# Kernel tuning notes

Measured on AMD Instinct MI355X. Metric: run time of the kernel, lower is better.

## Reference

```python
import jax, jax.numpy as jnp
import numpy as np

B, Q, P, HID, H, KV, D = 2, 1024, 3072, 4096, 32, 8, 128
G = H // KV          # GQA group size
EPS = 1e-6
ROPE_THETA = 1e6


def setup_inputs() -> dict:
    key = jax.random.key(0)
    ks = jax.random.split(key, 8)
    hidden_states = jax.random.normal(ks[0], (B, Q, HID), jnp.float32)
    # real RoPE tables for positions [P, P+Q) (extend phase)
    pos = jnp.arange(P, P + Q, dtype=jnp.float32)
    inv_freq = 1.0 / (ROPE_THETA ** (jnp.arange(0, D, 2, dtype=jnp.float32) / D))
    freqs = pos[:, None] * inv_freq[None, :]            # [Q, D/2]
    emb = jnp.concatenate([freqs, freqs], axis=-1)       # [Q, D]
    cos = jnp.broadcast_to(jnp.cos(emb)[None], (B, Q, D)).astype(jnp.float32)
    sin = jnp.broadcast_to(jnp.sin(emb)[None], (B, Q, D)).astype(jnp.float32)
    k_cache = jax.random.normal(ks[1], (B, KV, P, D), jnp.float32)
    v_cache = jax.random.normal(ks[2], (B, KV, P, D), jnp.float32)
    s = 0.02
    Wq = jax.random.normal(ks[3], (HID, H * D), jnp.float32) * s
    Wk = jax.random.normal(ks[4], (HID, KV * D), jnp.float32) * s
    Wv = jax.random.normal(ks[5], (HID, KV * D), jnp.float32) * s
    Wo = jax.random.normal(ks[6], (H * D, HID), jnp.float32) * s
    q_norm_w = jnp.ones((D,), jnp.float32)
    k_norm_w = jnp.ones((D,), jnp.float32)
    return dict(hidden_states=hidden_states, cos=cos, sin=sin,
                k_cache=k_cache, v_cache=v_cache,
                Wq=Wq, Wk=Wk, Wv=Wv, Wo=Wo,
                q_norm_w=q_norm_w, k_norm_w=k_norm_w)


def _rmsnorm(x, w):
    var = jnp.mean(x * x, axis=-1, keepdims=True)
    return x * jax.lax.rsqrt(var + EPS) * w


def _rotate_half(x):
    x1, x2 = jnp.split(x, 2, axis=-1)
    return jnp.concatenate([-x2, x1], axis=-1)


def _rope(x, cos, sin):
    # x: [B, h, Q, D]; cos/sin: [B, Q, D] -> broadcast over heads
    c = cos[:, None, :, :]
    s = sin[:, None, :, :]
    return x * c + _rotate_half(x) * s


def reference(hidden_states, cos, sin, k_cache, v_cache,
              Wq, Wk, Wv, Wo, q_norm_w, k_norm_w):
    # projections
    q = (hidden_states @ Wq).reshape(B, Q, H, D)
    k = (hidden_states @ Wk).reshape(B, Q, KV, D)
    v = (hidden_states @ Wv).reshape(B, Q, KV, D)
    # per-head RMSNorm on q and k
    q = _rmsnorm(q, q_norm_w)
    k = _rmsnorm(k, k_norm_w)
    # [B, heads, Q, D]
    q = q.transpose(0, 2, 1, 3)
    k = k.transpose(0, 2, 1, 3)
    v = v.transpose(0, 2, 1, 3)
    q = _rope(q, cos, sin)
    k = _rope(k, cos, sin)
    # extend: concat cached prefix KV with new KV -> kv_len = P + Q
    K = jnp.concatenate([k_cache, k], axis=2)   # [B, KV, P+Q, D]
    V = jnp.concatenate([v_cache, v], axis=2)
    qg = q.reshape(B, KV, G, Q, D)
    scale = 1.0 / jnp.sqrt(jnp.float32(D))
    scores = jnp.einsum('bkgqd,bksd->bkgqs', qg, K) * scale  # [B,KV,G,Q,P+Q]
    # causal mask offset by prefix: query i sees keys <= P + i
    key_idx = jnp.arange(P + Q)
    mask = key_idx[None, :] <= (P + jnp.arange(Q))[:, None]  # [Q, P+Q]
    scores = jnp.where(mask[None, None, None], scores, jnp.float32(-1e30))
    attn = jax.nn.softmax(scores, axis=-1)
    out = jnp.einsum('bkgqs,bksd->bkgqd', attn, V)           # [B,KV,G,Q,D]
    out = out.reshape(B, H, Q, D).transpose(0, 2, 1, 3).reshape(B, Q, H * D)
    return out @ Wo
```

## Files before the change

### kernel.cpp

```cpp
#include <hip/hip_runtime.h>
#include <hip/hip_bf16.h>

#define B_ 2
#define Q_ 1024
#define P_ 3072
#define HID_ 4096
#define H_ 32
#define KV_ 8
#define D_ 128
#define S_ 4096
#define NQKV 6144
#define QSCALE 0.1275174432f

typedef __attribute__((ext_vector_type(4))) float f32x4;
typedef __attribute__((ext_vector_type(8))) unsigned short u16x8;
typedef __attribute__((ext_vector_type(4))) unsigned short u16x4;
typedef __attribute__((ext_vector_type(8))) __bf16 bf16x8;

__device__ __forceinline__ unsigned short f2bf(float f){
  unsigned u = __builtin_bit_cast(unsigned, f);
  unsigned r = (u + 0x7FFFu + ((u >> 16) & 1u)) >> 16;
  return (unsigned short)r;
}
__device__ __forceinline__ unsigned pk2bf(float lo, float hi){
  unsigned r;
  asm("v_cvt_pk_bf16_f32 %0, %1, %2" : "=v"(r) : "v"(lo), "v"(hi));
  return r;
}
__device__ __forceinline__ f32x4 mfma16(u16x8 a, u16x8 b, f32x4 c){
  return __builtin_amdgcn_mfma_f32_16x16x32_bf16(
      __builtin_bit_cast(bf16x8, a), __builtin_bit_cast(bf16x8, b), c, 0, 0, 0);
}
typedef const __attribute__((address_space(1))) void* gp1_t;
typedef __attribute__((address_space(3))) void* lp3_t;
__device__ __forceinline__ void gl16(const unsigned short* g, unsigned short* l){
  __builtin_amdgcn_global_load_lds((gp1_t)g, (lp3_t)l, 16, 0, 0);
}

__global__ __launch_bounds__(256) void convert_hs(
    const float* __restrict__ X, unsigned short* __restrict__ Hh, int total4){
  for(int i4 = blockIdx.x * 256 + threadIdx.x; i4 < total4; i4 += gridDim.x * 256){
    long i = (long)i4 * 4;
    float4 x = *(const float4*)(X + i);
    *(u16x4*)(Hh + i) = (u16x4){f2bf(x.x), f2bf(x.y), f2bf(x.z), f2bf(x.w)};
  }
}

__global__ __launch_bounds__(256) void convert_wt(
    const float* __restrict__ W, unsigned short* __restrict__ Th, int ldn, int n_off){
  __shared__ float tile[64][65];
  int k0 = blockIdx.y * 64, n0 = blockIdx.x * 64;
  int tid = threadIdx.x;
  int r = tid >> 4, c = (tid & 15) * 4;
  #pragma unroll
  for(int j = 0; j < 4; ++j){
    float4 v = *(const float4*)(W + (long)(k0 + r + j*16) * ldn + n0 + c);
    tile[r + j*16][c] = v.x; tile[r + j*16][c+1] = v.y;
    tile[r + j*16][c+2] = v.z; tile[r + j*16][c+3] = v.w;
  }
  __syncthreads();
  #pragma unroll
  for(int j = 0; j < 4; ++j){
    int n = r + j*16;
    long o = (long)(n_off + n0 + n) * 4096 + k0 + c;
    *(u16x4*)(Th + o) = (u16x4){f2bf(tile[c][n]), f2bf(tile[c+1][n]),
                                f2bf(tile[c+2][n]), f2bf(tile[c+3][n])};
  }
}

__global__ __launch_bounds__(256) void cache_k(
    const float* __restrict__ kc, unsigned short* __restrict__ Kb){
  const int PD = P_ * D_;
  const long SD = (long)S_ * D_;
  int total4 = (B_ * KV_ * PD) >> 2;
  for(int i4 = blockIdx.x * 256 + threadIdx.x; i4 < total4; i4 += gridDim.x * 256){
    long i = (long)i4 * 4;
    int bkv = (int)(i / PD);
    int rem = (int)(i - (long)bkv * PD);
    long dst = (long)bkv * SD + rem;
    float4 k4 = *(const float4*)(kc + i);
    *(u16x4*)(Kb + dst) = (u16x4){f2bf(k4.x), f2bf(k4.y), f2bf(k4.z), f2bf(k4.w)};
  }
}

__global__ __launch_bounds__(256) void cache_vt(
    const float* __restrict__ vc, unsigned short* __restrict__ VT){
  __shared__ unsigned short T[128][72];
  int bkv = blockIdx.y;
  int s0 = blockIdx.x * 64;
  int tid = threadIdx.x;
  int r = tid >> 2, dblk = (tid & 3) * 32;
  const float* src = vc + ((long)bkv * P_ + s0 + r) * 128 + dblk;
  #pragma unroll
  for(int u = 0; u < 8; ++u){
    float4 v = *(const float4*)(src + u*4);
    T[dblk + u*4 + 0][r] = f2bf(v.x);
    T[dblk + u*4 + 1][r] = f2bf(v.y);
    T[dblk + u*4 + 2][r] = f2bf(v.z);
    T[dblk + u*4 + 3][r] = f2bf(v.w);
  }
  __syncthreads();
  int d = tid >> 1, sh = (tid & 1) * 32;
  unsigned short* dst = VT + ((long)bkv * 128 + d) * S_ + s0 + sh;
  #pragma unroll
  for(int u = 0; u < 4; ++u){
    u16x8 v;
    #pragma unroll
    for(int j = 0; j < 8; ++j) v[j] = T[d][sh + u*8 + j];
    *(u16x8*)(dst + u*8) = v;
  }
}

__global__ __launch_bounds__(128) void maxw(
    const float* __restrict__ qw, const float* __restrict__ kw, float* __restrict__ M){
  __shared__ float sa[2], sb[2];
  int t = threadIdx.x;
  float a = fabsf(qw[t]), b = fabsf(kw[t]);
  #pragma unroll
  for(int o = 32; o; o >>= 1){
    a = fmaxf(a, __shfl_xor(a, o));
    b = fmaxf(b, __shfl_xor(b, o));
  }
  if((t & 63) == 0){ sa[t >> 6] = a; sb[t >> 6] = b; }
  __syncthreads();
  if(t == 0){
    float mq = fmaxf(sa[0], sa[1]), mk = fmaxf(sb[0], sb[1]);
    M[0] = 128.0f * QSCALE * mq * mk * 1.01f + 0.25f;
  }
}

__global__ __launch_bounds__(256) void gemm_bf16(
    const unsigned short* __restrict__ Ag, const unsigned short* __restrict__ Bg,
    float* __restrict__ C, int nbx, int ldc){
  __shared__ __align__(16) unsigned short sA[4096], sB[4096];
  int tid = threadIdx.x;
  int nwg = nbx * 16;
  int lin = blockIdx.x;
  int cpx = nwg >> 3;
  int swz = (lin & 7) * cpx + (lin >> 3);
  int bx = swz % nbx, by = swz / nbx;
  int m0 = by * 128, n0 = bx * 128;
  int lane = tid & 63, w = tid >> 6;
  int lr = lane & 15, lg = lane >> 4;
  int wm = (w >> 1) * 64, wn = (w & 1) * 64;
  int rowi = w * 16 + (lane >> 2);
  int cchunk = ((lane & 3) ^ ((lane >> 3) & 3)) << 3;
  const unsigned short* aP = Ag + (long)(m0 + rowi) * 4096 + cchunk;
  const unsigned short* bP = Bg + (long)(n0 + rowi) * 4096 + cchunk;
  const int step2 = 64 * 4096;
  unsigned short* dA = sA + w * 512;
  unsigned short* dB = sB + w * 512;
  int rdcol = (lg * 8) ^ (((lr >> 1) & 3) << 3);
  f32x4 zero = {0.f,0.f,0.f,0.f};
  f32x4 acc[4][4];
  #pragma unroll
  for(int mi=0;mi<4;++mi)
    #pragma unroll
    for(int ni=0;ni<4;++ni) acc[mi][ni] = zero;

  for(int kt = 0; kt < 128; ++kt){
    int kk = kt * 32;
    __syncthreads();
    gl16(aP + kk, dA);  gl16(aP + step2 + kk, dA + 2048);
    gl16(bP + kk, dB);  gl16(bP + step2 + kk, dB + 2048);
    __syncthreads();
    u16x8 ah[4];
    #pragma unroll
    for(int mi = 0; mi < 4; ++mi)
      ah[mi] = *(const u16x8*)(sA + (wm + mi*16 + lr) * 32 + rdcol);
    #pragma unroll
    for(int ni = 0; ni < 4; ++ni){
      u16x8 bh = *(const u16x8*)(sB + (wn + ni*16 + lr) * 32 + rdcol);
      #pragma unroll
      for(int mi = 0; mi < 4; ++mi)
        acc[mi][ni] = mfma16(ah[mi], bh, acc[mi][ni]);
    }
  }
  #pragma unroll
  for(int mi = 0; mi < 4; ++mi)
    #pragma unroll
    for(int r = 0; r < 4; ++r){
      long rowoff = (long)(m0 + wm + mi*16 + lg*4 + r) * ldc + n0 + wn + lr;
      #pragma unroll
      for(int ni = 0; ni < 4; ++ni)
        C[rowoff + ni*16] = acc[mi][ni][r];
    }
}

__global__ __launch_bounds__(256) void pp_q(
    const float* __restrict__ Craw, const float* __restrict__ cosb,
    const float* __restrict__ sinb, const float* __restrict__ qw,
    unsigned short* __restrict__ Qb){
  int rid = blockIdx.x * 4 + (threadIdx.x >> 6);
  int lane = threadIdx.x & 63;
  int b = rid >> 15;
  int rem = rid & 32767;
  int q = rem >> 5;
  int h = rem & 31;
  long rowoff = (long)(b * Q_ + q) * NQKV + h * 128;
  float x1 = Craw[rowoff + lane];
  float x2 = Craw[rowoff + 64 + lane];
  float ss = x1*x1 + x2*x2;
  for(int o = 32; o; o >>= 1) ss += __shfl_xor(ss, o);
  float norm = rsqrtf(ss * (1.0f/128.0f) + 1e-6f);
  float xn1 = x1 * norm * qw[lane];
  float xn2 = x2 * norm * qw[64 + lane];
  long co = (long)(b * Q_ + q) * 128;
  float c1 = cosb[co + lane],      s1 = sinb[co + lane];
  float c2 = cosb[co + 64 + lane], s2 = sinb[co + 64 + lane];
  float o1 = (xn1 * c1 - xn2 * s1) * QSCALE;
  float o2 = (xn2 * c2 + xn1 * s2) * QSCALE;
  long dst = ((long)(b * H_ + h) * Q_ + q) * 128;
  Qb[dst + lane] = f2bf(o1);
  Qb[dst + 64 + lane] = f2bf(o2);
}

__global__ __launch_bounds__(256) void pp_kv(
    const float* __restrict__ Craw, const float* __restrict__ cosb,
    const float* __restrict__ sinb, const float* __restrict__ kw,
    unsigned short* __restrict__ Kb, unsigned short* __restrict__ VT){
  int rid = blockIdx.x * 4 + (threadIdx.x >> 6);
  int lane = threadIdx.x & 63;
  int b = rid >> 13;
  int rem = rid & 8191;
  int q = rem >> 3;
  int kv = rem & 7;
  int bkv = b * KV_ + kv;
  long rowoff = (long)(b * Q_ + q) * NQKV;
  float x1 = Craw[rowoff + 4096 + kv*128 + lane];
  float x2 = Craw[rowoff + 4096 + kv*128 + 64 + lane];
  float ss = x1*x1 + x2*x2;
  for(int o = 32; o; o >>= 1) ss += __shfl_xor(ss, o);
  float norm = rsqrtf(ss * (1.0f/128.0f) + 1e-6f);
  float xn1 = x1 * norm * kw[lane];
  float xn2 = x2 * norm * kw[64 + lane];
  long co = (long)(b * Q_ + q) * 128;
  float c1 = cosb[co + lane],      s1 = sinb[co + lane];
  float c2 = cosb[co + 64 + lane], s2 = sinb[co + 64 + lane];
  long dst = ((long)bkv * S_ + P_ + q) * 128;
  Kb[dst + lane]      = f2bf(xn1 * c1 - xn2 * s1);
  Kb[dst + 64 + lane] = f2bf(xn2 * c2 + xn1 * s2);
  float v1 = Craw[rowoff + 5120 + kv*128 + lane];
  float v2 = Craw[rowoff + 5120 + kv*128 + 64 + lane];
  VT[((long)bkv * 128 + lane) * S_ + P_ + q]      = f2bf(v1);
  VT[((long)bkv * 128 + 64 + lane) * S_ + P_ + q] = f2bf(v2);
}

#define KVB 32
#define PSL 40
__global__ __launch_bounds__(256) void attn(
    const unsigned short* __restrict__ Qg, const unsigned short* __restrict__ Kg,
    const unsigned short* __restrict__ VTg, const float* __restrict__ Mp,
    float* __restrict__ po, float* __restrict__ pl){
  __shared__ __align__(16) unsigned short Ks[2][KVB*128];
  __shared__ __align__(16) unsigned short Vs[2][128*KVB];
  __shared__ __align__(16) unsigned short Ps[4][32*PSL];
  int tid = threadIdx.x;
  int qb = blockIdx.x >> 1, sp = blockIdx.x & 1;
  int b = blockIdx.z, h = blockIdx.y, q0 = qb * 128;
  int kvh = h >> 2;
  int w = tid >> 6, lane = tid & 63, lr = lane & 15, lg = lane >> 4;
  int q0w = q0 + w * 32;
  float Mv = Mp[0];
  u16x8 qh[2][4];
  #pragma unroll
  for(int mi = 0; mi < 2; ++mi){
    long qbase = ((long)(b * H_ + h) * Q_ + q0w + mi*16 + lr) * 128;
    #pragma unroll
    for(int c = 0; c < 4; ++c)
      qh[mi][c] = *(const u16x8*)(Qg + qbase + c*32 + lg*8);
  }
  f32x4 minit = {-Mv, -Mv, -Mv, -Mv};
  f32x4 zero = {0.f,0.f,0.f,0.f};
  f32x4 o[2][8];
  #pragma unroll
  for(int mi = 0; mi < 2; ++mi)
    #pragma unroll
    for(int i = 0; i < 8; ++i) o[mi][i] = zero;
  float l[2] = {0.f, 0.f};
  long kb  = (long)(b * KV_ + kvh) * S_ * 128;
  long vb0 = (long)(b * KV_ + kvh) * 128 * (long)S_;
  int T = 100 + 4 * qb;
  int half = T >> 1;
  int t0 = sp ? half : 0;
  int t1 = sp ? T : half;
  int koff[2], voff[2], ldst[2];
  #pragma unroll
  for(int i = 0; i < 2; ++i){
    int L = (w*2 + i)*64 + lane;
    ldst[i] = L * 8;
    int r = L >> 4, c8 = (L & 15) ^ (r & 7);
    koff[i] = r*128 + c8*8;
    int d = L >> 2, sc = (L & 3) ^ (d & 3) ^ ((d >> 2) & 3);
    voff[i] = d*S_ + sc*8;
  }
  {
    const unsigned short* kg = Kg + kb + (long)t0 * (KVB*128);
    const unsigned short* vg = VTg + vb0 + t0 * KVB;
    #pragma unroll
    for(int i = 0; i < 2; ++i){
      gl16(kg + koff[i], &Ks[t0 & 1][ldst[i]]);
      gl16(vg + voff[i], &Vs[t0 & 1][ldst[i]]);
    }
  }
  __syncthreads();

  int lr7 = lr & 7;
  for(int t = t0; t < t1; ++t){
    int cur = t & 1;
    if(t + 1 < t1){
      int s1 = (t + 1) * KVB;
      const unsigned short* kg = Kg + kb + (long)s1 * 128;
      const unsigned short* vg = VTg + vb0 + s1;
      #pragma unroll
      for(int i = 0; i < 2; ++i){
        gl16(kg + koff[i], &Ks[cur^1][ldst[i]]);
        gl16(vg + voff[i], &Vs[cur^1][ldst[i]]);
      }
    }
    int s0 = t * KVB;
    if(s0 <= P_ + q0w + 31){
      f32x4 pacc[2][2];
      pacc[0][0] = minit; pacc[0][1] = minit; pacc[1][0] = minit; pacc[1][1] = minit;
      #pragma unroll
      for(int c = 0; c < 4; ++c)
        #pragma unroll
        for(int ni = 0; ni < 2; ++ni){
          u16x8 kh = *(const u16x8*)(&Ks[cur][(ni*16 + lr)*128 + (((c*4 + lg) ^ lr7) << 3)]);
          pacc[0][ni] = mfma16(kh, qh[0][c], pacc[0][ni]);
          pacc[1][ni] = mfma16(kh, qh[1][c], pacc[1][ni]);
        }
      if(s0 + KVB - 1 > P_ + q0w){
        #pragma unroll
        for(int mi = 0; mi < 2; ++mi){
          int qrow = q0w + mi*16 + lr;
          #pragma unroll
          for(int ni = 0; ni < 2; ++ni)
            #pragma unroll
            for(int r = 0; r < 4; ++r){
              int skey = s0 + ni*16 + lg*4 + r;
              if(skey > P_ + qrow) pacc[mi][ni][r] = -1e30f;
            }
        }
      }
      #pragma unroll
      for(int mi = 0; mi < 2; ++mi){
        float rs = 0.f;
        #pragma unroll
        for(int ni = 0; ni < 2; ++ni){
          float p0 = exp2f(pacc[mi][ni][0]);
          float p1 = exp2f(pacc[mi][ni][1]);
          float p2 = exp2f(pacc[mi][ni][2]);
          float p3 = exp2f(pacc[mi][ni][3]);
          rs += (p0 + p1) + (p2 + p3);
          uint2 pw; pw.x = pk2bf(p0, p1); pw.y = pk2bf(p2, p3);
          *(uint2*)(&Ps[w][(mi*16 + lr)*PSL + ni*16 + lg*4]) = pw;
        }
        l[mi] += rs;
      }
      u16x8 pa0 = *(const u16x8*)(&Ps[w][lr*PSL + lg*8]);
      u16x8 pa1 = *(const u16x8*)(&Ps[w][(16 + lr)*PSL + lg*8]);
      #pragma unroll
      for(int ni = 0; ni < 8; ++ni){
        int d = ni*16 + lr;
        int scs = lg ^ (lr & 3) ^ ((lr >> 2) & 3);
        u16x8 vbf = *(const u16x8*)(&Vs[cur][d*32 + (scs << 3)]);
        o[0][ni] = mfma16(pa0, vbf, o[0][ni]);
        o[1][ni] = mfma16(pa1, vbf, o[1][ni]);
      }
    }
    __syncthreads();
  }
  int bh = b * H_ + h;
  #pragma unroll
  for(int mi = 0; mi < 2; ++mi){
    float lt = l[mi];
    lt += __shfl_xor(lt, 16);
    lt += __shfl_xor(lt, 32);
    #pragma unroll
    for(int r = 0; r < 4; ++r){
      int qrow = q0w + mi*16 + lg*4 + r;
      long obase = ((long)(sp*64 + bh) * Q_ + qrow) * 128;
      #pragma unroll
      for(int ni = 0; ni < 8; ++ni)
        po[obase + ni*16 + lr] = o[mi][ni][r];
    }
    if(lane < 16)
      pl[(sp*64 + bh) * Q_ + q0w + mi*16 + lane] = lt;
  }
}

__global__ __launch_bounds__(256) void combine(
    const float* __restrict__ po, const float* __restrict__ pl,
    unsigned short* __restrict__ OH){
  int idx = blockIdx.x * 256 + threadIdx.x;
  int row = idx >> 5;
  int d4 = (idx & 31) * 4;
  int bh = row >> 10, q = row & 1023;
  int b = bh >> 5, h = bh & 31;
  float lsum = pl[bh*1024 + q] + pl[65536 + bh*1024 + q];
  float inv = 1.0f / lsum;
  float4 a = *(const float4*)(po + (long)row*128 + d4);
  float4 c = *(const float4*)(po + 8388608L + (long)row*128 + d4);
  u16x4 r = { f2bf((a.x + c.x) * inv), f2bf((a.y + c.y) * inv),
              f2bf((a.z + c.z) * inv), f2bf((a.w + c.w) * inv) };
  *(u16x4*)(OH + ((long)(b*1024 + q))*4096 + h*128 + d4) = r;
}

extern "C" void kernel_launch(void* const* d_in, const int* in_sizes, int n_in,
                              void* d_out, int out_size, void* d_ws, size_t ws_size,
                              hipStream_t stream){
  const float* hs   = (const float*)d_in[0];
  const float* cosb = (const float*)d_in[1];
  const float* sinb = (const float*)d_in[2];
  const float* kc   = (const float*)d_in[3];
  const float* vc   = (const float*)d_in[4];
  const float* Wq   = (const float*)d_in[5];
  const float* Wk   = (const float*)d_in[6];
  const float* Wv   = (const float*)d_in[7];
  const float* Wo   = (const float*)d_in[8];
  const float* qw   = (const float*)d_in[9];
  const float* kw   = (const float*)d_in[10];
  char* ws = (char*)d_ws;
  float* Craw          = (float*)ws;
  unsigned short* OH   = (unsigned short*)ws;
  float* PL            = (float*)(ws + 16777216);
  float* MW            = (float*)(ws + 17301504);
  unsigned short* WTh  = (unsigned short*)(ws + 50331648);
  unsigned short* WoTh = (unsigned short*)(ws + 50331648);
  float* PO            = (float*)(ws + 83886080);
  unsigned short* AH   = (unsigned short*)(ws + 150994944);
  unsigned short* QB   = (unsigned short*)(ws + 150994944);
  unsigned short* KB   = (unsigned short*)(ws + 184549376);
  unsigned short* VT   = (unsigned short*)(ws + 218103808);
  float* Out = (float*)d_out;

  convert_hs<<<dim3(2048), dim3(256), 0, stream>>>(hs, AH, (B_*Q_*HID_)/4);
  convert_wt<<<dim3(64,64), dim3(256), 0, stream>>>(Wq, WTh, 4096, 0);
  convert_wt<<<dim3(16,64), dim3(256), 0, stream>>>(Wk, WTh, 1024, 4096);
  convert_wt<<<dim3(16,64), dim3(256), 0, stream>>>(Wv, WTh, 1024, 5120);
  cache_k<<<dim3(2048), dim3(256), 0, stream>>>(kc, KB);
  cache_vt<<<dim3(48, 16), dim3(256), 0, stream>>>(vc, VT);
  gemm_bf16<<<dim3(768), dim3(256), 0, stream>>>(AH, WTh, Craw, 48, NQKV);
  pp_q<<<dim3(16384), dim3(256), 0, stream>>>(Craw, cosb, sinb, qw, QB);
  pp_kv<<<dim3(4096), dim3(256), 0, stream>>>(Craw, cosb, sinb, kw, KB, VT);
  maxw<<<dim3(1), dim3(128), 0, stream>>>(qw, kw, MW);
  convert_wt<<<dim3(64,64), dim3(256), 0, stream>>>(Wo, WoTh, 4096, 0);
  attn<<<dim3(16, 32, 2), dim3(256), 0, stream>>>(QB, KB, VT, MW, PO, PL);
  combine<<<dim3(8192), dim3(256), 0, stream>>>(PO, PL, OH);
  gemm_bf16<<<dim3(512), dim3(256), 0, stream>>>(OH, WoTh, Out, 32, 4096);
}
```

Baseline: 537.0 us.

## Merge prep kernels, enlarge attention query tile, add MFMA priority hints

Merges the hidden-state and K-cache conversions into one kernel, converts all four weight matrices in a single launch, and fuses the Q and KV post-processing kernels, cutting the launch count. The attention kernel now handles 64 query rows per wave (256 per block), so each K/V tile in shared memory serves twice as many queries, and it sets launch bounds for 2 blocks per CU. s_setprio hints are placed around the MFMA sections in both the GEMM and attention kernels. The workspace layout is repacked so that Wo can be converted early without clobbering other buffers. The larger attention tile raises register pressure and halves the grid, which may reduce occupancy and worsen the balance of the causal work.

```diff
diff --git a/kernel.cpp b/kernel.cpp
--- a/kernel.cpp
+++ b/kernel.cpp
@@ -37,19 +37,41 @@
   __builtin_amdgcn_global_load_lds((gp1_t)g, (lp3_t)l, 16, 0, 0);
 }
 
-__global__ __launch_bounds__(256) void convert_hs(
-    const float* __restrict__ X, unsigned short* __restrict__ Hh, int total4){
-  for(int i4 = blockIdx.x * 256 + threadIdx.x; i4 < total4; i4 += gridDim.x * 256){
-    long i = (long)i4 * 4;
-    float4 x = *(const float4*)(X + i);
-    *(u16x4*)(Hh + i) = (u16x4){f2bf(x.x), f2bf(x.y), f2bf(x.z), f2bf(x.w)};
-  }
-}
-
-__global__ __launch_bounds__(256) void convert_wt(
-    const float* __restrict__ W, unsigned short* __restrict__ Th, int ldn, int n_off){
+#define N1_ 2097152
+#define N2_ 1572864
+__global__ __launch_bounds__(256) void prep(
+    const float* __restrict__ hs, const float* __restrict__ kc,
+    unsigned short* __restrict__ AH, unsigned short* __restrict__ Kb){
+  const int PD = P_ * D_;
+  const long SD = (long)S_ * D_;
+  for(int i4 = blockIdx.x * 256 + threadIdx.x; i4 < N1_ + N2_; i4 += gridDim.x * 256){
+    if(i4 < N1_){
+      long i = (long)i4 * 4;
+      float4 x = *(const float4*)(hs + i);
+      *(u16x4*)(AH + i) = (u16x4){f2bf(x.x), f2bf(x.y), f2bf(x.z), f2bf(x.w)};
+    } else {
+      long i = (long)(i4 - N1_) * 4;
+      int bkv = (int)(i / PD);
+      int rem = (int)(i - (long)bkv * PD);
+      long dst = (long)bkv * SD + rem;
+      float4 k4 = *(const float4*)(kc + i);
+      *(u16x4*)(Kb + dst) = (u16x4){f2bf(k4.x), f2bf(k4.y), f2bf(k4.z), f2bf(k4.w)};
+    }
+  }
+}
+
+__global__ __launch_bounds__(256) void convert_w(
+    const float* __restrict__ Wq, const float* __restrict__ Wk,
+    const float* __restrict__ Wv, const float* __restrict__ Wo,
+    unsigned short* __restrict__ WT, unsigned short* __restrict__ WoT){
   __shared__ float tile[64][65];
-  int k0 = blockIdx.y * 64, n0 = blockIdx.x * 64;
+  int x = blockIdx.x;
+  const float* W; int ldn, n_off; unsigned short* dst; int n0;
+  if(x < 64)      { W = Wq; ldn = 4096; n_off = 0;    dst = WT;  n0 = x * 64; }
+  else if(x < 80) { W = Wk; ldn = 1024; n_off = 4096; dst = WT;  n0 = (x-64) * 64; }
+  else if(x < 96) { W = Wv; ldn = 1024; n_off = 5120; dst = WT;  n0 = (x-80) * 64; }
+  else            { W = Wo; ldn = 4096; n_off = 0;    dst = WoT; n0 = (x-96) * 64; }
+  int k0 = blockIdx.y * 64;
   int tid = threadIdx.x;
   int r = tid >> 4, c = (tid & 15) * 4;
   #pragma unroll
@@ -63,23 +85,8 @@
   for(int j = 0; j < 4; ++j){
     int n = r + j*16;
     long o = (long)(n_off + n0 + n) * 4096 + k0 + c;
-    *(u16x4*)(Th + o) = (u16x4){f2bf(tile[c][n]), f2bf(tile[c+1][n]),
-                                f2bf(tile[c+2][n]), f2bf(tile[c+3][n])};
-  }
-}
-
-__global__ __launch_bounds__(256) void cache_k(
-    const float* __restrict__ kc, unsigned short* __restrict__ Kb){
-  const int PD = P_ * D_;
-  const long SD = (long)S_ * D_;
-  int total4 = (B_ * KV_ * PD) >> 2;
-  for(int i4 = blockIdx.x * 256 + threadIdx.x; i4 < total4; i4 += gridDim.x * 256){
-    long i = (long)i4 * 4;
-    int bkv = (int)(i / PD);
-    int rem = (int)(i - (long)bkv * PD);
-    long dst = (long)bkv * SD + rem;
-    float4 k4 = *(const float4*)(kc + i);
-    *(u16x4*)(Kb + dst) = (u16x4){f2bf(k4.x), f2bf(k4.y), f2bf(k4.z), f2bf(k4.w)};
+    *(u16x4*)(dst + o) = (u16x4){f2bf(tile[c][n]), f2bf(tile[c+1][n]),
+                                 f2bf(tile[c+2][n]), f2bf(tile[c+3][n])};
   }
 }
 
@@ -168,6 +175,7 @@
     #pragma unroll
     for(int mi = 0; mi < 4; ++mi)
       ah[mi] = *(const u16x8*)(sA + (wm + mi*16 + lr) * 32 + rdcol);
+    __builtin_amdgcn_s_setprio(1);
     #pragma unroll
     for(int ni = 0; ni < 4; ++ni){
       u16x8 bh = *(const u16x8*)(sB + (wn + ni*16 + lr) * 32 + rdcol);
@@ -175,6 +183,7 @@
       for(int mi = 0; mi < 4; ++mi)
         acc[mi][ni] = mfma16(ah[mi], bh, acc[mi][ni]);
     }
+    __builtin_amdgcn_s_setprio(0);
   }
   #pragma unroll
   for(int mi = 0; mi < 4; ++mi)
@@ -187,84 +196,81 @@
     }
 }
 
-__global__ __launch_bounds__(256) void pp_q(
+__global__ __launch_bounds__(256) void pp_qkv(
     const float* __restrict__ Craw, const float* __restrict__ cosb,
     const float* __restrict__ sinb, const float* __restrict__ qw,
-    unsigned short* __restrict__ Qb){
-  int rid = blockIdx.x * 4 + (threadIdx.x >> 6);
-  int lane = threadIdx.x & 63;
-  int b = rid >> 15;
-  int rem = rid & 32767;
-  int q = rem >> 5;
-  int h = rem & 31;
-  long rowoff = (long)(b * Q_ + q) * NQKV + h * 128;
-  float x1 = Craw[rowoff + lane];
-  float x2 = Craw[rowoff + 64 + lane];
-  float ss = x1*x1 + x2*x2;
-  for(int o = 32; o; o >>= 1) ss += __shfl_xor(ss, o);
-  float norm = rsqrtf(ss * (1.0f/128.0f) + 1e-6f);
-  float xn1 = x1 * norm * qw[lane];
-  float xn2 = x2 * norm * qw[64 + lane];
-  long co = (long)(b * Q_ + q) * 128;
-  float c1 = cosb[co + lane],      s1 = sinb[co + lane];
-  float c2 = cosb[co + 64 + lane], s2 = sinb[co + 64 + lane];
-  float o1 = (xn1 * c1 - xn2 * s1) * QSCALE;
-  float o2 = (xn2 * c2 + xn1 * s2) * QSCALE;
-  long dst = ((long)(b * H_ + h) * Q_ + q) * 128;
-  Qb[dst + lane] = f2bf(o1);
-  Qb[dst + 64 + lane] = f2bf(o2);
-}
-
-__global__ __launch_bounds__(256) void pp_kv(
-    const float* __restrict__ Craw, const float* __restrict__ cosb,
-    const float* __restrict__ sinb, const float* __restrict__ kw,
+    const float* __restrict__ kw, unsigned short* __restrict__ Qb,
     unsigned short* __restrict__ Kb, unsigned short* __restrict__ VT){
   int rid = blockIdx.x * 4 + (threadIdx.x >> 6);
   int lane = threadIdx.x & 63;
-  int b = rid >> 13;
-  int rem = rid & 8191;
-  int q = rem >> 3;
-  int kv = rem & 7;
-  int bkv = b * KV_ + kv;
-  long rowoff = (long)(b * Q_ + q) * NQKV;
-  float x1 = Craw[rowoff + 4096 + kv*128 + lane];
-  float x2 = Craw[rowoff + 4096 + kv*128 + 64 + lane];
-  float ss = x1*x1 + x2*x2;
-  for(int o = 32; o; o >>= 1) ss += __shfl_xor(ss, o);
-  float norm = rsqrtf(ss * (1.0f/128.0f) + 1e-6f);
-  float xn1 = x1 * norm * kw[lane];
-  float xn2 = x2 * norm * kw[64 + lane];
-  long co = (long)(b * Q_ + q) * 128;
-  float c1 = cosb[co + lane],      s1 = sinb[co + lane];
-  float c2 = cosb[co + 64 + lane], s2 = sinb[co + 64 + lane];
-  long dst = ((long)bkv * S_ + P_ + q) * 128;
-  Kb[dst + lane]      = f2bf(xn1 * c1 - xn2 * s1);
-  Kb[dst + 64 + lane] = f2bf(xn2 * c2 + xn1 * s2);
-  float v1 = Craw[rowoff + 5120 + kv*128 + lane];
-  float v2 = Craw[rowoff + 5120 + kv*128 + 64 + lane];
-  VT[((long)bkv * 128 + lane) * S_ + P_ + q]      = f2bf(v1);
-  VT[((long)bkv * 128 + 64 + lane) * S_ + P_ + q] = f2bf(v2);
+  if(rid < 65536){
+    int b = rid >> 15;
+    int rem = rid & 32767;
+    int q = rem >> 5;
+    int h = rem & 31;
+    long rowoff = (long)(b * Q_ + q) * NQKV + h * 128;
+    float x1 = Craw[rowoff + lane];
+    float x2 = Craw[rowoff + 64 + lane];
+    float ss = x1*x1 + x2*x2;
+    for(int o = 32; o; o >>= 1) ss += __shfl_xor(ss, o);
+    float norm = rsqrtf(ss * (1.0f/128.0f) + 1e-6f);
+    float xn1 = x1 * norm * qw[lane];
+    float xn2 = x2 * norm * qw[64 + lane];
+    long co = (long)(b * Q_ + q) * 128;
+    float c1 = cosb[co + lane],      s1 = sinb[co + lane];
+    float c2 = cosb[co + 64 + lane], s2 = sinb[co + 64 + lane];
+    float o1 = (xn1 * c1 - xn2 * s1) * QSCALE;
+    float o2 = (xn2 * c2 + xn1 * s2) * QSCALE;
+    long dst = ((long)(b * H_ + h) * Q_ + q) * 128;
+    Qb[dst + lane] = f2bf(o1);
+    Qb[dst + 64 + lane] = f2bf(o2);
+  } else {
+    int rid2 = rid - 65536;
+    int b = rid2 >> 13;
+    int rem = rid2 & 8191;
+    int q = rem >> 3;
+    int kv = rem & 7;
+    int bkv = b * KV_ + kv;
+    long rowoff = (long)(b * Q_ + q) * NQKV;
+    float x1 = Craw[rowoff + 4096 + kv*128 + lane];
+    float x2 = Craw[rowoff + 4096 + kv*128 + 64 + lane];
+    float ss = x1*x1 + x2*x2;
+    for(int o = 32; o; o >>= 1) ss += __shfl_xor(ss, o);
+    float norm = rsqrtf(ss * (1.0f/128.0f) + 1e-6f);
+    float xn1 = x1 * norm * kw[lane];
+    float xn2 = x2 * norm * kw[64 + lane];
+    long co = (long)(b * Q_ + q) * 128;
+    float c1 = cosb[co + lane],      s1 = sinb[co + lane];
+    float c2 = cosb[co + 64 + lane], s2 = sinb[co + 64 + lane];
+    long dst = ((long)bkv * S_ + P_ + q) * 128;
+    Kb[dst + lane]      = f2bf(xn1 * c1 - xn2 * s1);
+    Kb[dst + 64 + lane] = f2bf(xn2 * c2 + xn1 * s2);
+    float v1 = Craw[rowoff + 5120 + kv*128 + lane];
+    float v2 = Craw[rowoff + 5120 + kv*128 + 64 + lane];
+    VT[((long)bkv * 128 + lane) * S_ + P_ + q]      = f2bf(v1);
+    VT[((long)bkv * 128 + 64 + lane) * S_ + P_ + q] = f2bf(v2);
+  }
 }
 
 #define KVB 32
 #define PSL 40
-__global__ __launch_bounds__(256) void attn(
+__global__ __launch_bounds__(256, 2) void attn(
     const unsigned short* __restrict__ Qg, const unsigned short* __restrict__ Kg,
     const unsigned short* __restrict__ VTg, const float* __restrict__ Mp,
     float* __restrict__ po, float* __restrict__ pl){
   __shared__ __align__(16) unsigned short Ks[2][KVB*128];
   __shared__ __align__(16) unsigned short Vs[2][128*KVB];
-  __shared__ __align__(16) unsigned short Ps[4][32*PSL];
+  __shared__ __align__(16) unsigned short Ps[4][64*PSL];
   int tid = threadIdx.x;
   int qb = blockIdx.x >> 1, sp = blockIdx.x & 1;
-  int b = blockIdx.z, h = blockIdx.y, q0 = qb * 128;
+  int b = blockIdx.z, h = blockIdx.y, q0 = qb * 256;
   int kvh = h >> 2;
   int w = tid >> 6, lane = tid & 63, lr = lane & 15, lg = lane >> 4;
-  int q0w = q0 + w * 32;
+  int q0w = q0 + w * 64;
   float Mv = Mp[0];
-  u16x8 qh[2][4];
-  #pragma unroll
-  for(int mi = 0; mi < 2; ++mi){
+  u16x8 qh[4][4];
+  #pragma unroll
+  for(int mi = 0; mi < 4; ++mi){
     long qbase = ((long)(b * H_ + h) * Q_ + q0w + mi*16 + lr) * 128;
     #pragma unroll
     for(int c = 0; c < 4; ++c)
@@ -272,15 +278,15 @@
   }
   f32x4 minit = {-Mv, -Mv, -Mv, -Mv};
   f32x4 zero = {0.f,0.f,0.f,0.f};
-  f32x4 o[2][8];
-  #pragma unroll
-  for(int mi = 0; mi < 2; ++mi)
+  f32x4 o[4][8];
+  #pragma unroll
+  for(int mi = 0; mi < 4; ++mi)
     #pragma unroll
     for(int i = 0; i < 8; ++i) o[mi][i] = zero;
-  float l[2] = {0.f, 0.f};
+  float l[4] = {0.f, 0.f, 0.f, 0.f};
   long kb  = (long)(b * KV_ + kvh) * S_ * 128;
   long vb0 = (long)(b * KV_ + kvh) * 128 * (long)S_;
-  int T = 100 + 4 * qb;
+  int T = 104 + 8 * qb;
   int half = T >> 1;
   int t0 = sp ? half : 0;
   int t1 = sp ? T : half;
@@ -319,20 +325,24 @@
       }
     }
     int s0 = t * KVB;
-    if(s0 <= P_ + q0w + 31){
-      f32x4 pacc[2][2];
-      pacc[0][0] = minit; pacc[0][1] = minit; pacc[1][0] = minit; pacc[1][1] = minit;
+    if(s0 <= P_ + q0w + 63){
+      f32x4 pacc[4][2];
+      #pragma unroll
+      for(int mi = 0; mi < 4; ++mi){ pacc[mi][0] = minit; pacc[mi][1] = minit; }
+      __builtin_amdgcn_s_setprio(1);
       #pragma unroll
       for(int c = 0; c < 4; ++c)
         #pragma unroll
         for(int ni = 0; ni < 2; ++ni){
           u16x8 kh = *(const u16x8*)(&Ks[cur][(ni*16 + lr)*128 + (((c*4 + lg) ^ lr7) << 3)]);
-          pacc[0][ni] = mfma16(kh, qh[0][c], pacc[0][ni]);
-          pacc[1][ni] = mfma16(kh, qh[1][c], pacc[1][ni]);
+          #pragma unroll
+          for(int mi = 0; mi < 4; ++mi)
+            pacc[mi][ni] = mfma16(kh, qh[mi][c], pacc[mi][ni]);
         }
+      __builtin_amdgcn_s_setprio(0);
       if(s0 + KVB - 1 > P_ + q0w){
         #pragma unroll
-        for(int mi = 0; mi < 2; ++mi){
+        for(int mi = 0; mi < 4; ++mi){
           int qrow = q0w + mi*16 + lr;
           #pragma unroll
           for(int ni = 0; ni < 2; ++ni)
@@ -344,7 +354,7 @@
         }
       }
       #pragma unroll
-      for(int mi = 0; mi < 2; ++mi){
+      for(int mi = 0; mi < 4; ++mi){
         float rs = 0.f;
         #pragma unroll
         for(int ni = 0; ni < 2; ++ni){
@@ -358,22 +368,27 @@
         }
         l[mi] += rs;
       }
-      u16x8 pa0 = *(const u16x8*)(&Ps[w][lr*PSL + lg*8]);
-      u16x8 pa1 = *(const u16x8*)(&Ps[w][(16 + lr)*PSL + lg*8]);
+      u16x8 pa[4];
+      #pragma unroll
+      for(int mi = 0; mi < 4; ++mi)
+        pa[mi] = *(const u16x8*)(&Ps[w][(mi*16 + lr)*PSL + lg*8]);
+      __builtin_amdgcn_s_setprio(1);
       #pragma unroll
       for(int ni = 0; ni < 8; ++ni){
         int d = ni*16 + lr;
         int scs = lg ^ (lr & 3) ^ ((lr >> 2) & 3);
         u16x8 vbf = *(const u16x8*)(&Vs[cur][d*32 + (scs << 3)]);
-        o[0][ni] = mfma16(pa0, vbf, o[0][ni]);
-        o[1][ni] = mfma16(pa1, vbf, o[1][ni]);
+        #pragma unroll
+        for(int mi = 0; mi < 4; ++mi)
+          o[mi][ni] = mfma16(pa[mi], vbf, o[mi][ni]);
       }
+      __builtin_amdgcn_s_setprio(0);
     }
     __syncthreads();
   }
   int bh = b * H_ + h;
   #pragma unroll
-  for(int mi = 0; mi < 2; ++mi){
+  for(int mi = 0; mi < 4; ++mi){
     float lt = l[mi];
     lt += __shfl_xor(lt, 16);
     lt += __shfl_xor(lt, 32);
@@ -424,29 +439,24 @@
   char* ws = (char*)d_ws;
   float* Craw          = (float*)ws;
   unsigned short* OH   = (unsigned short*)ws;
-  float* PL            = (float*)(ws + 16777216);
-  float* MW            = (float*)(ws + 17301504);
-  unsigned short* WTh  = (unsigned short*)(ws + 50331648);
-  unsigned short* WoTh = (unsigned short*)(ws + 50331648);
-  float* PO            = (float*)(ws + 83886080);
+  unsigned short* WT   = (unsigned short*)(ws + 50331648);
+  float* PO            = (float*)(ws + 50331648);
+  unsigned short* WoT  = (unsigned short*)(ws + 117440512);
   unsigned short* AH   = (unsigned short*)(ws + 150994944);
   unsigned short* QB   = (unsigned short*)(ws + 150994944);
-  unsigned short* KB   = (unsigned short*)(ws + 184549376);
-  unsigned short* VT   = (unsigned short*)(ws + 218103808);
+  unsigned short* KB   = (unsigned short*)(ws + 167772160);
+  unsigned short* VT   = (unsigned short*)(ws + 184549376);
+  float* PL            = (float*)(ws + 201326592);
+  float* MW            = (float*)(ws + 201981952);
   float* Out = (float*)d_out;
 
-  convert_hs<<<dim3(2048), dim3(256), 0, stream>>>(hs, AH, (B_*Q_*HID_)/4);
-  convert_wt<<<dim3(64,64), dim3(256), 0, stream>>>(Wq, WTh, 4096, 0);
-  convert_wt<<<dim3(16,64), dim3(256), 0, stream>>>(Wk, WTh, 1024, 4096);
-  convert_wt<<<dim3(16,64), dim3(256), 0, stream>>>(Wv, WTh, 1024, 5120);
-  cache_k<<<dim3(2048), dim3(256), 0, stream>>>(kc, KB);
+  prep<<<dim3(2048), dim3(256), 0, stream>>>(hs, kc, AH, KB);
+  convert_w<<<dim3(160, 64), dim3(256), 0, stream>>>(Wq, Wk, Wv, Wo, WT, WoT);
   cache_vt<<<dim3(48, 16), dim3(256), 0, stream>>>(vc, VT);
-  gemm_bf16<<<dim3(768), dim3(256), 0, stream>>>(AH, WTh, Craw, 48, NQKV);
-  pp_q<<<dim3(16384), dim3(256), 0, stream>>>(Craw, cosb, sinb, qw, QB);
-  pp_kv<<<dim3(4096), dim3(256), 0, stream>>>(Craw, cosb, sinb, kw, KB, VT);
   maxw<<<dim3(1), dim3(128), 0, stream>>>(qw, kw, MW);
-  convert_wt<<<dim3(64,64), dim3(256), 0, stream>>>(Wo, WoTh, 4096, 0);
-  attn<<<dim3(16, 32, 2), dim3(256), 0, stream>>>(QB, KB, VT, MW, PO, PL);
+  gemm_bf16<<<dim3(768), dim3(256), 0, stream>>>(AH, WT, Craw, 48, NQKV);
+  pp_qkv<<<dim3(20480), dim3(256), 0, stream>>>(Craw, cosb, sinb, qw, kw, QB, KB, VT);
+  attn<<<dim3(8, 32, 2), dim3(256), 0, stream>>>(QB, KB, VT, MW, PO, PL);
   combine<<<dim3(8192), dim3(256), 0, stream>>>(PO, PL, OH);
-  gemm_bf16<<<dim3(512), dim3(256), 0, stream>>>(OH, WoTh, Out, 32, 4096);
-}
+  gemm_bf16<<<dim3(512), dim3(256), 0, stream>>>(OH, WoT, Out, 32, 4096);
+}
```

Measured after the change: 604.3 us. 1.13x slower.
